# Kernel tuning notes

Hardware: AMD Instinct MI355X
Metric: run time of the kernel (lower is better)

## Reference

```python
import jax, jax.numpy as jnp
import numpy as np

N = 50000      # nodes
E = 800000     # edges (before self loops)
HID = 128      # hidden_dim
FEAT = 128     # feat_dim
NEG_SLOPE = 0.2
BN_EPS = 1e-5


def setup_inputs() -> dict:
    key = jax.random.key(0)
    ks = jax.random.split(key, 16)
    s = lambda d: 1.0 / np.sqrt(d).astype(np.float32)
    return {
        "x": jax.random.normal(ks[0], (N, HID), jnp.float32),
        "edge_index": jax.random.randint(ks[1], (2, E), 0, N, jnp.int32),
        # GATConv 1 (hidden -> hidden)
        "W1": jax.random.normal(ks[2], (HID, HID), jnp.float32) * s(HID),
        "att_src1": jax.random.normal(ks[3], (HID,), jnp.float32) * s(HID),
        "att_dst1": jax.random.normal(ks[4], (HID,), jnp.float32) * s(HID),
        "b1": jnp.zeros((HID,), jnp.float32),
        # BatchNorm1d(hidden) -- eval mode buffers/params
        "bn_gamma": jnp.ones((HID,), jnp.float32),
        "bn_beta": jnp.zeros((HID,), jnp.float32),
        "bn_mean": jax.random.normal(ks[5], (HID,), jnp.float32) * 0.1,
        "bn_var": jax.random.uniform(ks[6], (HID,), jnp.float32, 0.5, 1.5),
        # GATConv 2 (hidden -> feat)
        "W2": jax.random.normal(ks[7], (HID, FEAT), jnp.float32) * s(HID),
        "att_src2": jax.random.normal(ks[8], (FEAT,), jnp.float32) * s(FEAT),
        "att_dst2": jax.random.normal(ks[9], (FEAT,), jnp.float32) * s(FEAT),
        "b2": jnp.zeros((FEAT,), jnp.float32),
    }


def _gat_conv(x, W, att_src, att_dst, bias, src, dst, n_nodes):
    """PyG GATConv, heads=1: gather -> edge attn -> segment softmax -> scatter."""
    h = x @ W                                   # [N, d_out]
    a_s = h @ att_src                           # [N]
    a_d = h @ att_dst                           # [N]
    e = jax.nn.leaky_relu(a_s[src] + a_d[dst], NEG_SLOPE)  # [E']
    # numerically-stable softmax over incoming edges of each dst node
    e_max = jax.ops.segment_max(e, dst, num_segments=n_nodes)
    ex = jnp.exp(e - e_max[dst])
    denom = jax.ops.segment_sum(ex, dst, num_segments=n_nodes)
    alpha = ex / (denom[dst] + 1e-16)           # [E']
    out = jax.ops.segment_sum(alpha[:, None] * h[src], dst, num_segments=n_nodes)
    return out + bias


def reference(x, edge_index, W1, att_src1, att_dst1, b1,
              bn_gamma, bn_beta, bn_mean, bn_var,
              W2, att_src2, att_dst2, b2):
    n = x.shape[0]
    loops = jnp.arange(n, dtype=edge_index.dtype)
    src = jnp.concatenate([edge_index[0], loops])
    dst = jnp.concatenate([edge_index[1], loops])

    h = jax.nn.relu(_gat_conv(x, W1, att_src1, att_dst1, b1, src, dst, n))
    # BatchNorm1d in eval mode (running stats); dropout is identity in eval
    h = (h - bn_mean) * jax.lax.rsqrt(bn_var + BN_EPS) * bn_gamma + bn_beta
    out = jax.nn.relu(_gat_conv(h, W2, att_src2, att_dst2, b2, src, dst, n))
    return out
```

## Files before the change

kernel.cpp:

```cpp
#include <hip/hip_runtime.h>

typedef unsigned short u16;
typedef unsigned int   u32;
typedef __attribute__((ext_vector_type(8))) short bh8;
typedef __attribute__((ext_vector_type(4))) float fx4;

__device__ __forceinline__ float b2f(u16 h){ return __uint_as_float(((u32)h) << 16); }
__device__ __forceinline__ u16   f2b(float f){
  u32 u = __float_as_uint(f);
  u32 r = u + 0x7FFFu + ((u >> 16) & 1u);
  return (u16)(r >> 16);
}
__device__ __forceinline__ float lo16(u32 w){ return b2f((u16)(w & 0xFFFFu)); }
__device__ __forceinline__ float hi16(u32 w){ return b2f((u16)(w >> 16)); }

__global__ void r21_zero(int* p, int n){
  int t = blockIdx.x*blockDim.x + threadIdx.x;
  if (t < n) p[t] = 0;
}

__global__ void r21_hist_prep(const int* __restrict__ ei, int E, int Ep, int* cnt,
                              u16* __restrict__ rank,
                              const float* __restrict__ W1, const float* __restrict__ as1,
                              const float* __restrict__ ad1,
                              const float* __restrict__ W2, const float* __restrict__ as2,
                              const float* __restrict__ ad2,
                              u16* __restrict__ w1H, u16* __restrict__ w1L,
                              u16* __restrict__ w2H, u16* __restrict__ w2L,
                              float* __restrict__ ws1, float* __restrict__ wd1,
                              float* __restrict__ ws2, float* __restrict__ wd2){
  int b = blockIdx.x;
  int t = threadIdx.x;
  if (b < 16){
    const float* W = (b < 8) ? W1 : W2;
    u16* HT = (b < 8) ? w1H : w2H;
    u16* LT = (b < 8) ? w1L : w2L;
    int n0 = (b & 7) * 16;
    #pragma unroll
    for (int it = 0; it < 8; ++it){
      int idx = it*256 + t;
      int nn = n0 + (idx >> 7);
      int k = idx & 127;
      float w = W[(size_t)k*128 + nn];
      u16 h = f2b(w);
      HT[(size_t)nn*128 + k] = h;
      LT[(size_t)nn*128 + k] = f2b(w - b2f(h));
    }
    return;
  }
  if (b == 16){
    int which = t >> 6;
    const float* W   = (which < 2) ? W1 : W2;
    const float* att = (which == 0) ? as1 : (which == 1) ? ad1 : (which == 2) ? as2 : ad2;
    float* outv      = (which == 0) ? ws1 : (which == 1) ? wd1 : (which == 2) ? ws2 : wd2;
    int k0 = (t & 63) * 2;
    #pragma unroll
    for (int kk = 0; kk < 2; ++kk){
      int k = k0 + kk;
      float s = 0.f;
      for (int c = 0; c < 128; ++c) s = fmaf(W[(size_t)k*128 + c], att[c], s);
      outv[k] = s;
    }
    return;
  }
  int g0 = (b - 17)*1024 + t;
  #pragma unroll
  for (int i = 0; i < 4; ++i){
    int g = g0 + i*256;
    if (g < Ep){
      int dst = (g < E) ? ei[E + g] : (g - E);
      int r = atomicAdd(&cnt[dst], 1);
      rank[g] = (u16)r;
    }
  }
}

__global__ void r21_scan1(const int* in, int n, int* incl, int* bsums){
  __shared__ int tmp[256];
  int t = threadIdx.x; int g = blockIdx.x*256 + t;
  int v = (g < n) ? in[g] : 0;
  tmp[t] = v; __syncthreads();
  for (int off = 1; off < 256; off <<= 1){
    int u = (t >= off) ? tmp[t - off] : 0;
    __syncthreads();
    tmp[t] += u;
    __syncthreads();
  }
  if (g < n) incl[g] = tmp[t];
  if (t == 255) bsums[blockIdx.x] = tmp[255];
}

__global__ void r21_scan2(int* bsums, int nb){
  __shared__ int tmp[256];
  int t = threadIdx.x;
  int v = (t < nb) ? bsums[t] : 0;
  tmp[t] = v; __syncthreads();
  for (int off = 1; off < 256; off <<= 1){
    int u = (t >= off) ? tmp[t - off] : 0;
    __syncthreads();
    tmp[t] += u;
    __syncthreads();
  }
  if (t < nb) bsums[t] = tmp[t];
}

__global__ void r21_scan3(const int* incl, const int* cnt, const int* bsums,
                          int n, int* offs){
  int t = threadIdx.x; int b = blockIdx.x; int g = b*256 + t;
  if (g >= n) return;
  int add = (b > 0) ? bsums[b-1] : 0;
  offs[g] = incl[g] - cnt[g] + add;
}

__device__ __forceinline__ void gemm16_wave(
    const float* __restrict__ X, const u16* __restrict__ wH, const u16* __restrict__ wL,
    const float* __restrict__ wsv, const float* __restrict__ wdv,
    u16* __restrict__ HB, float* __restrict__ AS, float* __restrict__ AD,
    int nrows, int w, int lane)
{
  int r0 = w * 16;
  if (r0 >= nrows) return;
  int rloc = lane & 15;
  int q    = lane >> 4;
  int myrow = r0 + rloc;
  bool act = (myrow < nrows);
  int rsafe = act ? myrow : (nrows - 1);

  fx4 acc[8] = {};
  float ds = 0.f, dd = 0.f;

  const u16* wHrow = wH + (size_t)rloc * 128;
  const u16* wLrow = wL + (size_t)rloc * 128;

  #pragma unroll
  for (int kk = 0; kk < 4; ++kk){
    int kbase = kk*32 + q*8;
    const float* xp = X + (size_t)rsafe*128 + kbase;
    float4 xa = *(const float4*)xp;
    float4 xb = *(const float4*)(xp + 4);
    float xv[8] = {xa.x, xa.y, xa.z, xa.w, xb.x, xb.y, xb.z, xb.w};
    if (!act){
      #pragma unroll
      for (int i = 0; i < 8; ++i) xv[i] = 0.f;
    }
    const float* sp = wsv + kbase;
    const float* dp = wdv + kbase;
    bh8 xh, xl;
    #pragma unroll
    for (int i = 0; i < 8; ++i){
      ds = fmaf(xv[i], sp[i], ds);
      dd = fmaf(xv[i], dp[i], dd);
      u16 h = f2b(xv[i]);
      xh[i] = (short)h;
      xl[i] = (short)f2b(xv[i] - b2f(h));
    }
    #pragma unroll
    for (int cf = 0; cf < 8; ++cf){
      bh8 wh = *(const bh8*)(wHrow + (size_t)cf*2048 + kbase);
      bh8 wl = *(const bh8*)(wLrow + (size_t)cf*2048 + kbase);
      acc[cf] = __builtin_amdgcn_mfma_f32_16x16x32_bf16(wh, xh, acc[cf], 0, 0, 0);
      acc[cf] = __builtin_amdgcn_mfma_f32_16x16x32_bf16(wl, xh, acc[cf], 0, 0, 0);
      acc[cf] = __builtin_amdgcn_mfma_f32_16x16x32_bf16(wh, xl, acc[cf], 0, 0, 0);
    }
  }
  ds += __shfl_xor(ds, 16); ds += __shfl_xor(ds, 32);
  dd += __shfl_xor(dd, 16); dd += __shfl_xor(dd, 32);
  if (act && q == 0){ AS[myrow] = ds; AD[myrow] = dd; }
  if (act){
    u16* hrow = HB + (size_t)myrow*128 + q*4;
    #pragma unroll
    for (int cf = 0; cf < 8; ++cf){
      uint2 pb;
      pb.x = (u32)f2b(acc[cf][0]) | ((u32)f2b(acc[cf][1]) << 16);
      pb.y = (u32)f2b(acc[cf][2]) | ((u32)f2b(acc[cf][3]) << 16);
      *(uint2*)(hrow + cf*16) = pb;
    }
  }
}

__global__ __launch_bounds__(256)
void r21_gemm_fill(const float* __restrict__ X,
                   const u16* __restrict__ wH, const u16* __restrict__ wL,
                   const float* __restrict__ wsv, const float* __restrict__ wdv,
                   u16* __restrict__ HB, float* __restrict__ AS, float* __restrict__ AD,
                   int nrows, int gemmBlocks,
                   const int* __restrict__ ei, int E, int Ep,
                   const int* __restrict__ offs, const u16* __restrict__ rank,
                   u16* __restrict__ csr){
  int t = threadIdx.x;
  if ((int)blockIdx.x >= gemmBlocks){
    int g0 = ((int)blockIdx.x - gemmBlocks)*1024 + t;
    #pragma unroll
    for (int i = 0; i < 4; ++i){
      int g = g0 + i*256;
      if (g < Ep){
        int src, dst;
        if (g < E){ src = ei[g]; dst = ei[E + g]; } else { src = g - E; dst = g - E; }
        csr[offs[dst] + (int)rank[g]] = (u16)src;
      }
    }
    return;
  }
  int w = (int)blockIdx.x*4 + (t >> 6);
  gemm16_wave(X, wH, wL, wsv, wdv, HB, AS, AD, nrows, w, t & 63);
}

__global__ __launch_bounds__(256)
void r21_gemm(const float* __restrict__ X,
              const u16* __restrict__ wH, const u16* __restrict__ wL,
              const float* __restrict__ wsv, const float* __restrict__ wdv,
              u16* __restrict__ HB, float* __restrict__ AS, float* __restrict__ AD,
              int nrows){
  int w = (int)blockIdx.x*4 + (threadIdx.x >> 6);
  gemm16_wave(X, wH, wL, wsv, wdv, HB, AS, AD, nrows, w, threadIdx.x & 63);
}

__global__ __launch_bounds__(256)
void r21_aggregate(const u16* __restrict__ HB, const float* __restrict__ AS,
                   const float* __restrict__ AD,
                   const int* __restrict__ offs, const u16* __restrict__ csr,
                   const float* __restrict__ bias,
                   const float* __restrict__ gamma_, const float* __restrict__ beta_,
                   const float* __restrict__ mean_, const float* __restrict__ var_,
                   float* __restrict__ outp, int n, int doBN){
  int wid  = (blockIdx.x*256 + threadIdx.x) >> 6;
  int lane = threadIdx.x & 63;
  if (wid >= n) return;
  int beg = offs[wid], end = offs[wid+1];
  int deg = end - beg;
  float ad = AD[wid];
  int h  = lane >> 5;
  int c4 = (lane & 31) * 4;
  float a0 = 0.f, a1 = 0.f, a2 = 0.f, a3 = 0.f;

  if (deg <= 64){
    int   my_s = 0;
    float my_e = -3.0e38f;
    bool act = (lane < deg);
    if (act){
      my_s = (int)csr[beg + lane];
      float e = AS[my_s] + ad;
      my_e = (e > 0.f) ? e : 0.2f*e;
    }
    float m = my_e;
    #pragma unroll
    for (int off = 32; off >= 1; off >>= 1) m = fmaxf(m, __shfl_xor(m, off));
    float pz = act ? __expf(my_e - m) : 0.f;
    float den = pz;
    #pragma unroll
    for (int off = 32; off >= 1; off >>= 1) den += __shfl_xor(den, off);
    float my_al = pz / (den + 1e-16f);

    int npair = (deg + 1) >> 1;
    int k = 0;
    for (; k + 8 <= npair; k += 8){
      int j0 = 2*k + h;
      int   s0 = __shfl(my_s, j0),    s1 = __shfl(my_s, j0+2);
      int   s2 = __shfl(my_s, j0+4),  s3 = __shfl(my_s, j0+6);
      int   s4 = __shfl(my_s, j0+8),  s5 = __shfl(my_s, j0+10);
      int   s6 = __shfl(my_s, j0+12), s7 = __shfl(my_s, j0+14);
      float l0 = __shfl(my_al, j0),    l1 = __shfl(my_al, j0+2);
      float l2 = __shfl(my_al, j0+4),  l3 = __shfl(my_al, j0+6);
      float l4 = __shfl(my_al, j0+8),  l5 = __shfl(my_al, j0+10);
      float l6 = __shfl(my_al, j0+12), l7 = __shfl(my_al, j0+14);
      uint2 q0 = *(const uint2*)&HB[(size_t)s0*128 + c4];
      uint2 q1 = *(const uint2*)&HB[(size_t)s1*128 + c4];
      uint2 q2 = *(const uint2*)&HB[(size_t)s2*128 + c4];
      uint2 q3 = *(const uint2*)&HB[(size_t)s3*128 + c4];
      uint2 q4 = *(const uint2*)&HB[(size_t)s4*128 + c4];
      uint2 q5 = *(const uint2*)&HB[(size_t)s5*128 + c4];
      uint2 q6 = *(const uint2*)&HB[(size_t)s6*128 + c4];
      uint2 q7 = *(const uint2*)&HB[(size_t)s7*128 + c4];
      a0 = fmaf(l0, lo16(q0.x), a0); a1 = fmaf(l0, hi16(q0.x), a1);
      a2 = fmaf(l0, lo16(q0.y), a2); a3 = fmaf(l0, hi16(q0.y), a3);
      a0 = fmaf(l1, lo16(q1.x), a0); a1 = fmaf(l1, hi16(q1.x), a1);
      a2 = fmaf(l1, lo16(q1.y), a2); a3 = fmaf(l1, hi16(q1.y), a3);
      a0 = fmaf(l2, lo16(q2.x), a0); a1 = fmaf(l2, hi16(q2.x), a1);
      a2 = fmaf(l2, lo16(q2.y), a2); a3 = fmaf(l2, hi16(q2.y), a3);
      a0 = fmaf(l3, lo16(q3.x), a0); a1 = fmaf(l3, hi16(q3.x), a1);
      a2 = fmaf(l3, lo16(q3.y), a2); a3 = fmaf(l3, hi16(q3.y), a3);
      a0 = fmaf(l4, lo16(q4.x), a0); a1 = fmaf(l4, hi16(q4.x), a1);
      a2 = fmaf(l4, lo16(q4.y), a2); a3 = fmaf(l4, hi16(q4.y), a3);
      a0 = fmaf(l5, lo16(q5.x), a0); a1 = fmaf(l5, hi16(q5.x), a1);
      a2 = fmaf(l5, lo16(q5.y), a2); a3 = fmaf(l5, hi16(q5.y), a3);
      a0 = fmaf(l6, lo16(q6.x), a0); a1 = fmaf(l6, hi16(q6.x), a1);
      a2 = fmaf(l6, lo16(q6.y), a2); a3 = fmaf(l6, hi16(q6.y), a3);
      a0 = fmaf(l7, lo16(q7.x), a0); a1 = fmaf(l7, hi16(q7.x), a1);
      a2 = fmaf(l7, lo16(q7.y), a2); a3 = fmaf(l7, hi16(q7.y), a3);
    }
    for (; k + 4 <= npair; k += 4){
      int j0 = 2*k + h, j1 = j0 + 2, j2 = j0 + 4, j3 = j0 + 6;
      int   s0 = __shfl(my_s, j0),  s1 = __shfl(my_s, j1);
      int   s2 = __shfl(my_s, j2),  s3 = __shfl(my_s, j3);
      float l0 = __shfl(my_al, j0), l1 = __shfl(my_al, j1);
      float l2 = __shfl(my_al, j2), l3 = __shfl(my_al, j3);
      uint2 q0 = *(const uint2*)&HB[(size_t)s0*128 + c4];
      uint2 q1 = *(const uint2*)&HB[(size_t)s1*128 + c4];
      uint2 q2 = *(const uint2*)&HB[(size_t)s2*128 + c4];
      uint2 q3 = *(const uint2*)&HB[(size_t)s3*128 + c4];
      a0 = fmaf(l0, lo16(q0.x), a0); a1 = fmaf(l0, hi16(q0.x), a1);
      a2 = fmaf(l0, lo16(q0.y), a2); a3 = fmaf(l0, hi16(q0.y), a3);
      a0 = fmaf(l1, lo16(q1.x), a0); a1 = fmaf(l1, hi16(q1.x), a1);
      a2 = fmaf(l1, lo16(q1.y), a2); a3 = fmaf(l1, hi16(q1.y), a3);
      a0 = fmaf(l2, lo16(q2.x), a0); a1 = fmaf(l2, hi16(q2.x), a1);
      a2 = fmaf(l2, lo16(q2.y), a2); a3 = fmaf(l2, hi16(q2.y), a3);
      a0 = fmaf(l3, lo16(q3.x), a0); a1 = fmaf(l3, hi16(q3.x), a1);
      a2 = fmaf(l3, lo16(q3.y), a2); a3 = fmaf(l3, hi16(q3.y), a3);
    }
    for (; k < npair; ++k){
      int j = 2*k + h;
      int   s = __shfl(my_s, j);
      float l = __shfl(my_al, j);
      uint2 q = *(const uint2*)&HB[(size_t)s*128 + c4];
      a0 = fmaf(l, lo16(q.x), a0); a1 = fmaf(l, hi16(q.x), a1);
      a2 = fmaf(l, lo16(q.y), a2); a3 = fmaf(l, hi16(q.y), a3);
    }
  } else {
    float m = -3.0e38f;
    for (int k = beg + lane; k < end; k += 64){
      int s = (int)csr[k];
      float e = AS[s] + ad; e = (e > 0.f) ? e : 0.2f*e;
      m = fmaxf(m, e);
    }
    #pragma unroll
    for (int off = 32; off >= 1; off >>= 1) m = fmaxf(m, __shfl_xor(m, off));
    float den = 0.f;
    for (int k = beg + lane; k < end; k += 64){
      int s = (int)csr[k];
      float e = AS[s] + ad; e = (e > 0.f) ? e : 0.2f*e;
      den += __expf(e - m);
    }
    #pragma unroll
    for (int off = 32; off >= 1; off >>= 1) den += __shfl_xor(den, off);
    float inv = 1.0f / (den + 1e-16f);
    for (int j = h; j < deg; j += 2){
      int s = (int)csr[beg + j];
      float e = AS[s] + ad; e = (e > 0.f) ? e : 0.2f*e;
      float al = __expf(e - m) * inv;
      uint2 q = *(const uint2*)&HB[(size_t)s*128 + c4];
      a0 = fmaf(al, lo16(q.x), a0); a1 = fmaf(al, hi16(q.x), a1);
      a2 = fmaf(al, lo16(q.y), a2); a3 = fmaf(al, hi16(q.y), a3);
    }
  }

  a0 += __shfl_xor(a0, 32); a1 += __shfl_xor(a1, 32);
  a2 += __shfl_xor(a2, 32); a3 += __shfl_xor(a3, 32);
  if (lane < 32){
    float4 bv = *(const float4*)(bias + c4);
    float v0 = fmaxf(a0 + bv.x, 0.f);
    float v1 = fmaxf(a1 + bv.y, 0.f);
    float v2 = fmaxf(a2 + bv.z, 0.f);
    float v3 = fmaxf(a3 + bv.w, 0.f);
    if (doBN){
      float4 gv = *(const float4*)(gamma_ + c4);
      float4 vv = *(const float4*)(var_   + c4);
      float4 mv = *(const float4*)(mean_  + c4);
      float4 be = *(const float4*)(beta_  + c4);
      v0 = (v0 - mv.x) * (gv.x * rsqrtf(vv.x + 1e-5f)) + be.x;
      v1 = (v1 - mv.y) * (gv.y * rsqrtf(vv.y + 1e-5f)) + be.y;
      v2 = (v2 - mv.z) * (gv.z * rsqrtf(vv.z + 1e-5f)) + be.z;
      v3 = (v3 - mv.w) * (gv.w * rsqrtf(vv.w + 1e-5f)) + be.w;
    }
    float4 o = {v0, v1, v2, v3};
    *(float4*)(outp + (size_t)wid*128 + c4) = o;
  }
}

extern "C" void kernel_launch(void* const* d_in, const int* in_sizes, int n_in,
                              void* d_out, int out_size, void* d_ws, size_t ws_size,
                              hipStream_t stream){
  const float* x   = (const float*)d_in[0];
  const int*   ei  = (const int*)  d_in[1];
  const float* W1  = (const float*)d_in[2];
  const float* as1 = (const float*)d_in[3];
  const float* ad1 = (const float*)d_in[4];
  const float* b1  = (const float*)d_in[5];
  const float* bng = (const float*)d_in[6];
  const float* bnb = (const float*)d_in[7];
  const float* bnm = (const float*)d_in[8];
  const float* bnv = (const float*)d_in[9];
  const float* W2  = (const float*)d_in[10];
  const float* as2 = (const float*)d_in[11];
  const float* ad2 = (const float*)d_in[12];
  const float* b2  = (const float*)d_in[13];
  float* out = (float*)d_out;

  int N  = in_sizes[0] / 128;
  int E  = in_sizes[1] / 2;
  int Ep = E + N;
  if (N <= 0 || E <= 0) return;

  char* base = (char*)d_ws;
  size_t off = 0;
  auto alloc = [&](size_t bytes)->char*{
    off = (off + 255) & ~(size_t)255;
    char* q = base + off; off += bytes; return q;
  };
  float* AS     = (float*)alloc((size_t)N*4);
  float* AD     = (float*)alloc((size_t)N*4);
  int*   cnt    = (int*)  alloc((size_t)(N+1)*4);
  int*   offs   = (int*)  alloc((size_t)(N+1)*4);
  int*   bsums  = (int*)  alloc(1024);
  u16*   rank   = (u16*)  alloc((size_t)Ep*2);
  u16*   csr    = (u16*)  alloc((size_t)Ep*2);
  u16*   hb     = (u16*)  alloc((size_t)N*128*2);
  float* x2     = (float*)alloc((size_t)N*128*4);
  u16*   w1H    = (u16*)  alloc(128*128*2);
  u16*   w1L    = (u16*)  alloc(128*128*2);
  u16*   w2H    = (u16*)  alloc(128*128*2);
  u16*   w2L    = (u16*)  alloc(128*128*2);
  float* ws1    = (float*)alloc(128*4);
  float* wd1    = (float*)alloc(128*4);
  float* ws2    = (float*)alloc(128*4);
  float* wd2    = (float*)alloc(128*4);

  int n1  = N + 1;
  int zb  = (n1 + 255)/256;
  int sb  = (n1 + 255)/256;
  int ebH = (Ep + 1023)/1024;
  int nW  = (N + 15)/16;
  int gwb = (nW + 3)/4;
  int wb  = (N + 3)/4;

  r21_zero     <<<zb, 256, 0, stream>>>(cnt, n1);
  r21_hist_prep<<<ebH + 17, 256, 0, stream>>>(ei, E, Ep, cnt, rank,
                                              W1, as1, ad1, W2, as2, ad2,
                                              w1H, w1L, w2H, w2L,
                                              ws1, wd1, ws2, wd2);
  r21_scan1    <<<sb, 256, 0, stream>>>(cnt, n1, offs, bsums);
  r21_scan2    <<<1, 256, 0, stream>>>(bsums, sb);
  r21_scan3    <<<sb, 256, 0, stream>>>(offs, cnt, bsums, n1, offs);
  r21_gemm_fill<<<gwb + ebH, 256, 0, stream>>>(x, w1H, w1L, ws1, wd1,
                                               hb, AS, AD, N, gwb,
                                               ei, E, Ep, offs, rank, csr);
  r21_aggregate<<<wb, 256, 0, stream>>>(hb, AS, AD, offs, csr, b1, bng, bnb, bnm, bnv,
                                        x2, N, 1);
  r21_gemm     <<<gwb, 256, 0, stream>>>(x2, w2H, w2L, ws2, wd2, hb, AS, AD, N);
  r21_aggregate<<<wb, 256, 0, stream>>>(hb, AS, AD, offs, csr, b2, 0, 0, 0, 0,
                                        out, N, 0);
}
```

Baseline: 310.2 us.

## Merge zeroing into prep, overlap histogram with GEMM, single-pass lookback scan

Folds the counter zeroing into the weight-prep kernel and moves the degree histogram (atomic ranks) into the first GEMM launch. The CSR fill becomes its own kernel. The three-kernel prefix scan is replaced by one kernel in which each block publishes its flagged total and spins on the totals of earlier blocks. The aim is fewer launches and overlapping the atomic histogram with the GEMM. The spin-wait relies on earlier blocks being scheduled first, which holds for about 196 blocks but is a forward-progress risk.

```diff
diff --git a/kernel.cpp b/kernel.cpp
--- a/kernel.cpp
+++ b/kernel.cpp
@@ -4,6 +4,8 @@
 typedef unsigned int   u32;
 typedef __attribute__((ext_vector_type(8))) short bh8;
 typedef __attribute__((ext_vector_type(4))) float fx4;
+
+#define SCAN_FLAG 0x40000000
 
 __device__ __forceinline__ float b2f(u16 h){ return __uint_as_float(((u32)h) << 16); }
 __device__ __forceinline__ u16   f2b(float f){
@@ -14,21 +16,15 @@
 __device__ __forceinline__ float lo16(u32 w){ return b2f((u16)(w & 0xFFFFu)); }
 __device__ __forceinline__ float hi16(u32 w){ return b2f((u16)(w >> 16)); }
 
-__global__ void r21_zero(int* p, int n){
-  int t = blockIdx.x*blockDim.x + threadIdx.x;
-  if (t < n) p[t] = 0;
-}
-
-__global__ void r21_hist_prep(const int* __restrict__ ei, int E, int Ep, int* cnt,
-                              u16* __restrict__ rank,
-                              const float* __restrict__ W1, const float* __restrict__ as1,
+__global__ void r22_prep_zero(const float* __restrict__ W1, const float* __restrict__ as1,
                               const float* __restrict__ ad1,
                               const float* __restrict__ W2, const float* __restrict__ as2,
                               const float* __restrict__ ad2,
                               u16* __restrict__ w1H, u16* __restrict__ w1L,
                               u16* __restrict__ w2H, u16* __restrict__ w2L,
                               float* __restrict__ ws1, float* __restrict__ wd1,
-                              float* __restrict__ ws2, float* __restrict__ wd2){
+                              float* __restrict__ ws2, float* __restrict__ wd2,
+                              int* __restrict__ cnt, int n1, int* __restrict__ pub){
   int b = blockIdx.x;
   int t = threadIdx.x;
   if (b < 16){
@@ -63,53 +59,9 @@
     }
     return;
   }
-  int g0 = (b - 17)*1024 + t;
-  #pragma unroll
-  for (int i = 0; i < 4; ++i){
-    int g = g0 + i*256;
-    if (g < Ep){
-      int dst = (g < E) ? ei[E + g] : (g - E);
-      int r = atomicAdd(&cnt[dst], 1);
-      rank[g] = (u16)r;
-    }
-  }
-}
-
-__global__ void r21_scan1(const int* in, int n, int* incl, int* bsums){
-  __shared__ int tmp[256];
-  int t = threadIdx.x; int g = blockIdx.x*256 + t;
-  int v = (g < n) ? in[g] : 0;
-  tmp[t] = v; __syncthreads();
-  for (int off = 1; off < 256; off <<= 1){
-    int u = (t >= off) ? tmp[t - off] : 0;
-    __syncthreads();
-    tmp[t] += u;
-    __syncthreads();
-  }
-  if (g < n) incl[g] = tmp[t];
-  if (t == 255) bsums[blockIdx.x] = tmp[255];
-}
-
-__global__ void r21_scan2(int* bsums, int nb){
-  __shared__ int tmp[256];
-  int t = threadIdx.x;
-  int v = (t < nb) ? bsums[t] : 0;
-  tmp[t] = v; __syncthreads();
-  for (int off = 1; off < 256; off <<= 1){
-    int u = (t >= off) ? tmp[t - off] : 0;
-    __syncthreads();
-    tmp[t] += u;
-    __syncthreads();
-  }
-  if (t < nb) bsums[t] = tmp[t];
-}
-
-__global__ void r21_scan3(const int* incl, const int* cnt, const int* bsums,
-                          int n, int* offs){
-  int t = threadIdx.x; int b = blockIdx.x; int g = b*256 + t;
-  if (g >= n) return;
-  int add = (b > 0) ? bsums[b-1] : 0;
-  offs[g] = incl[g] - cnt[g] + add;
+  int g = (b - 17)*256 + t;
+  if (g < n1) cnt[g] = 0;
+  else if (g < n1 + 256) pub[g - n1] = 0;
 }
 
 __device__ __forceinline__ void gemm16_wave(
@@ -179,14 +131,13 @@
 }
 
 __global__ __launch_bounds__(256)
-void r21_gemm_fill(const float* __restrict__ X,
+void r22_gemm_hist(const float* __restrict__ X,
                    const u16* __restrict__ wH, const u16* __restrict__ wL,
                    const float* __restrict__ wsv, const float* __restrict__ wdv,
                    u16* __restrict__ HB, float* __restrict__ AS, float* __restrict__ AD,
                    int nrows, int gemmBlocks,
                    const int* __restrict__ ei, int E, int Ep,
-                   const int* __restrict__ offs, const u16* __restrict__ rank,
-                   u16* __restrict__ csr){
+                   int* __restrict__ cnt, u16* __restrict__ rank){
   int t = threadIdx.x;
   if ((int)blockIdx.x >= gemmBlocks){
     int g0 = ((int)blockIdx.x - gemmBlocks)*1024 + t;
@@ -194,9 +145,9 @@
     for (int i = 0; i < 4; ++i){
       int g = g0 + i*256;
       if (g < Ep){
-        int src, dst;
-        if (g < E){ src = ei[g]; dst = ei[E + g]; } else { src = g - E; dst = g - E; }
-        csr[offs[dst] + (int)rank[g]] = (u16)src;
+        int dst = (g < E) ? ei[E + g] : (g - E);
+        int r = atomicAdd(&cnt[dst], 1);
+        rank[g] = (u16)r;
       }
     }
     return;
@@ -206,7 +157,55 @@
 }
 
 __global__ __launch_bounds__(256)
-void r21_gemm(const float* __restrict__ X,
+void r22_scan(const int* __restrict__ cnt, int n, int* __restrict__ offs,
+              int* __restrict__ pub){
+  __shared__ int tmp[256];
+  __shared__ int red[256];
+  int t = threadIdx.x; int b = blockIdx.x; int g = b*256 + t;
+  int v = (g < n) ? cnt[g] : 0;
+  tmp[t] = v; __syncthreads();
+  for (int off = 1; off < 256; off <<= 1){
+    int u = (t >= off) ? tmp[t - off] : 0;
+    __syncthreads();
+    tmp[t] += u;
+    __syncthreads();
+  }
+  int incl = tmp[t];
+  if (t == 255) atomicExch(&pub[b], tmp[255] | SCAN_FLAG);
+  int val = 0;
+  if (t < b){
+    int p;
+    do { p = atomicAdd(&pub[t], 0); } while (!(p & SCAN_FLAG));
+    val = p & ~SCAN_FLAG;
+  }
+  red[t] = val; __syncthreads();
+  for (int off = 128; off >= 1; off >>= 1){
+    if (t < off) red[t] += red[t + off];
+    __syncthreads();
+  }
+  int add = red[0];
+  if (g < n) offs[g] = add + incl - v;
+}
+
+__global__ __launch_bounds__(256)
+void r22_fill(const int* __restrict__ ei, int E, int Ep,
+              const int* __restrict__ offs, const u16* __restrict__ rank,
+              u16* __restrict__ csr){
+  int t = threadIdx.x;
+  int g0 = (int)blockIdx.x*1024 + t;
+  #pragma unroll
+  for (int i = 0; i < 4; ++i){
+    int g = g0 + i*256;
+    if (g < Ep){
+      int src, dst;
+      if (g < E){ src = ei[g]; dst = ei[E + g]; } else { src = g - E; dst = g - E; }
+      csr[offs[dst] + (int)rank[g]] = (u16)src;
+    }
+  }
+}
+
+__global__ __launch_bounds__(256)
+void r22_gemm(const float* __restrict__ X,
               const u16* __restrict__ wH, const u16* __restrict__ wL,
               const float* __restrict__ wsv, const float* __restrict__ wdv,
               u16* __restrict__ HB, float* __restrict__ AS, float* __restrict__ AD,
@@ -216,7 +215,7 @@
 }
 
 __global__ __launch_bounds__(256)
-void r21_aggregate(const u16* __restrict__ HB, const float* __restrict__ AS,
+void r22_aggregate(const u16* __restrict__ HB, const float* __restrict__ AS,
                    const float* __restrict__ AD,
                    const int* __restrict__ offs, const u16* __restrict__ csr,
                    const float* __restrict__ bias,
@@ -400,7 +399,7 @@
   float* AD     = (float*)alloc((size_t)N*4);
   int*   cnt    = (int*)  alloc((size_t)(N+1)*4);
   int*   offs   = (int*)  alloc((size_t)(N+1)*4);
-  int*   bsums  = (int*)  alloc(1024);
+  int*   pub    = (int*)  alloc(256*4);
   u16*   rank   = (u16*)  alloc((size_t)Ep*2);
   u16*   csr    = (u16*)  alloc((size_t)Ep*2);
   u16*   hb     = (u16*)  alloc((size_t)N*128*2);
@@ -415,27 +414,24 @@
   float* wd2    = (float*)alloc(128*4);
 
   int n1  = N + 1;
-  int zb  = (n1 + 255)/256;
   int sb  = (n1 + 255)/256;
+  int zb  = (n1 + 256 + 255)/256;
   int ebH = (Ep + 1023)/1024;
   int nW  = (N + 15)/16;
   int gwb = (nW + 3)/4;
   int wb  = (N + 3)/4;
 
-  r21_zero     <<<zb, 256, 0, stream>>>(cnt, n1);
-  r21_hist_prep<<<ebH + 17, 256, 0, stream>>>(ei, E, Ep, cnt, rank,
-                                              W1, as1, ad1, W2, as2, ad2,
-                                              w1H, w1L, w2H, w2L,
-                                              ws1, wd1, ws2, wd2);
-  r21_scan1    <<<sb, 256, 0, stream>>>(cnt, n1, offs, bsums);
-  r21_scan2    <<<1, 256, 0, stream>>>(bsums, sb);
-  r21_scan3    <<<sb, 256, 0, stream>>>(offs, cnt, bsums, n1, offs);
-  r21_gemm_fill<<<gwb + ebH, 256, 0, stream>>>(x, w1H, w1L, ws1, wd1,
+  r22_prep_zero<<<17 + zb, 256, 0, stream>>>(W1, as1, ad1, W2, as2, ad2,
+                                             w1H, w1L, w2H, w2L,
+                                             ws1, wd1, ws2, wd2, cnt, n1, pub);
+  r22_gemm_hist<<<gwb + ebH, 256, 0, stream>>>(x, w1H, w1L, ws1, wd1,
                                                hb, AS, AD, N, gwb,
-                                               ei, E, Ep, offs, rank, csr);
-  r21_aggregate<<<wb, 256, 0, stream>>>(hb, AS, AD, offs, csr, b1, bng, bnb, bnm, bnv,
+                                               ei, E, Ep, cnt, rank);
+  r22_scan<<<sb, 256, 0, stream>>>(cnt, n1, offs, pub);
+  r22_fill<<<ebH, 256, 0, stream>>>(ei, E, Ep, offs, rank, csr);
+  r22_aggregate<<<wb, 256, 0, stream>>>(hb, AS, AD, offs, csr, b1, bng, bnb, bnm, bnv,
                                         x2, N, 1);
-  r21_gemm     <<<gwb, 256, 0, stream>>>(x2, w2H, w2L, ws2, wd2, hb, AS, AD, N);
-  r21_aggregate<<<wb, 256, 0, stream>>>(hb, AS, AD, offs, csr, b2, 0, 0, 0, 0,
+  r22_gemm     <<<gwb, 256, 0, stream>>>(x2, w2H, w2L, ws2, wd2, hb, AS, AD, N);
+  r22_aggregate<<<wb, 256, 0, stream>>>(hb, AS, AD, offs, csr, b2, 0, 0, 0, 0,
                                         out, N, 0);
 }
```

Result: slower. 326.0 us (+5.1%).
